# Kernel optimization log

Hardware: AMD Instinct MI355X
Metric: run time of the kernel (lower is better)

## Reference

```python
import jax, jax.numpy as jnp
import numpy as np
from jax import lax

B, T, H, W, C = 2, 32, 65, 65, 32
KS = 15   # kernel_size
F = 32    # conv features


def setup_inputs() -> dict:
    key = jax.random.key(0)
    ks = jax.random.split(key, 12)
    d = {}
    d["input_seq"] = jax.random.normal(ks[0], (B, T, H, W, C), jnp.float32)
    d["conv_w"] = jax.random.normal(ks[1], (3, 3, C, F), jnp.float32) / np.sqrt(3 * 3 * C).astype(np.float32)
    d["conv_b"] = jnp.zeros((F,), jnp.float32)
    for i, nm in enumerate(["alpha", "delta", "mu", "gamma"]):
        d[f"w_{nm}"] = jax.random.normal(ks[2 + i], (F, C), jnp.float32) / np.sqrt(F).astype(np.float32)
        d[f"b_{nm}"] = jnp.zeros((C,), jnp.float32)
    # nn.initializers.normal() -> stddev 0.01
    d["k_exc"] = jax.random.normal(ks[10], (KS, KS, C), jnp.float32) * 0.01
    d["k_inh"] = jax.random.normal(ks[11], (KS, KS, C), jnp.float32) * 0.01
    return d


def _kernel_spec(k, Hh, Ww):
    # zero-pad the (KS,KS,C) kernel to (H,W,C), then rfft2 over spatial axes
    ph, pw = (Hh - KS) // 2, (Ww - KS) // 2
    kp = jnp.pad(k, ((ph, ph), (pw, pw), (0, 0)))
    return jnp.fft.rfft2(kp, axes=(0, 1))  # (H, W//2+1, C) complex64


def reference(input_seq, conv_w, conv_b, w_alpha, b_alpha, w_delta, b_delta,
              w_mu, b_mu, w_gamma, b_gamma, k_exc, k_inh):
    Bb, Tt, Hh, Ww, Cc = input_seq.shape
    # context conv: flax Conv flattens leading (B,T) into batch; SAME, stride 2
    x = input_seq.reshape(Bb * Tt, Hh, Ww, Cc)
    stats = lax.conv_general_dilated(x, conv_w, (2, 2), 'SAME',
                                     dimension_numbers=('NHWC', 'HWIO', 'NHWC')) + conv_b
    stats = jax.nn.gelu(stats)  # flax nn.gelu (approximate)
    Hp, Wp = stats.shape[1], stats.shape[2]
    stats = stats.reshape(Bb, Tt, Hp, Wp, F)
    ctx = jnp.mean(stats, axis=(1, 2))                 # (B, Wp, F); Wp == W//2+1 for odd W
    alpha = jax.nn.sigmoid(ctx @ w_alpha + b_alpha)    # (B, Wp, C)
    delta = jax.nn.sigmoid(ctx @ w_delta + b_delta)
    mu = jax.nn.softplus(ctx @ w_mu + b_mu)
    gamma = jax.nn.softplus(ctx @ w_gamma + b_gamma)

    K_E = _kernel_spec(k_exc, Hh, Ww)  # (H, Wr, C)
    K_I = _kernel_spec(k_inh, Hh, Ww)
    Wr = Ww // 2 + 1
    decay = jnp.asarray(0.9, jnp.complex64)

    bc = lambda v: jnp.broadcast_to(v[:, None, :, :].astype(jnp.complex64), (Bb, Hh, Wr, Cc))
    A_xx = decay * bc(alpha)
    A_yy = decay * bc(delta)
    A_xy = -K_I[None] * bc(mu)
    A_yx = K_E[None] * bc(gamma)
    row0 = jnp.stack([A_xx, A_xy], axis=-1)
    row1 = jnp.stack([A_yx, A_yy], axis=-1)
    K_hat = jnp.stack([row0, row1], axis=-2)           # (B, H, Wr, C, 2, 2)

    U_hat = jnp.fft.rfft2(input_seq, axes=(2, 3))      # (B, T, H, Wr, C) complex64
    U_vec = jnp.stack([U_hat, jnp.zeros_like(U_hat)], axis=-1)  # (B,T,H,Wr,C,2)
    A_t = jnp.broadcast_to(K_hat[:, None], (Bb, Tt, Hh, Wr, Cc, 2, 2))

    # associative op for linear SSM: state_t = A_t @ state_{t-1} + u_t
    # (log/exp of the original cancel: exp(log A)=A, exp(State_log)=State)
    def combine(l, r):
        A1, b1 = l
        A2, b2 = r
        A = jnp.einsum('...ij,...jk->...ik', A2, A1)
        b = jnp.einsum('...ij,...j->...i', A2, b1) + b2
        return A, b

    _, S = lax.associative_scan(combine, (A_t, U_vec), axis=1)
    Y = S[..., 1]                                      # inhibitory component
    return jnp.fft.irfft2(Y, axes=(2, 3))              # (B, T, H, 2*(Wr-1), C) float32
```

## Files before the change

### kernel.cpp

```cpp
#include <hip/hip_runtime.h>
#include <cmath>

#define NB 2
#define NT 32
#define NH 65
#define NW 65
#define NC 32
#define NF 32
#define NKS 15
#define NHP 33
#define NWP 33
#define NWR 33
#define NWOUT 64
#define PI_F 3.14159265358979323846f

using bf16x8 = __attribute__((ext_vector_type(8))) __bf16;
using f32x4  = __attribute__((ext_vector_type(4))) float;
using s16x4  = __attribute__((ext_vector_type(4))) short;

__device__ inline unsigned short f2bf(float v) {
    unsigned u = __float_as_uint(v);
    u = u + 0x7FFF + ((u >> 16) & 1);
    return (unsigned short)(u >> 16);
}
__device__ inline float bf2f(unsigned short h) {
    return __uint_as_float((unsigned)h << 16);
}

union FragU { s16x4 h[2]; bf16x8 v; };

__global__ __launch_bounds__(256) void setup_kernel(
    const float* __restrict__ w, unsigned short* __restrict__ wBh,
    unsigned short* __restrict__ wBl,
    float2* __restrict__ twr, float2* __restrict__ twb, float2* __restrict__ twi,
    const float* __restrict__ kexc, const float* __restrict__ kinh,
    float2* __restrict__ KE, float2* __restrict__ KI)
{
    int blk = blockIdx.x;
    if (blk < 10) {
        int tid = blk * 256 + threadIdx.x;
        if (tid < NH * 36) {
            int q = tid / 36, wr = tid % 36;
            float2 v = make_float2(0.f, 0.f);
            if (wr < NWR) {
                int p = (q * wr) % NH;
                float a = -2.f * PI_F * (float)p / (float)NH;
                v = make_float2(cosf(a), sinf(a));
            }
            twr[tid] = v;
        }
        if (tid < NH * 14) {
            int h = tid / 14, b = tid % 14;
            float2 v = make_float2(0.f, 0.f);
            if (b < 13) {
                int p = (h * b) % NH;
                float a = 2.f * PI_F * (float)p / (float)NH;
                v = make_float2(cosf(a), sinf(a));
            }
            twb[tid] = v;
        }
        if (tid < 31 * 64) {
            int q = tid / 64 + 1, ow = tid % 64;
            int p = (q * ow) & 63;
            float a = 2.f * PI_F * (float)p / (float)NWOUT;
            twi[tid] = make_float2(cosf(a), sinf(a));
        }
    } else if (blk < 46) {
        int tid = (blk - 10) * 256 + threadIdx.x;
        if (tid < 9 * NF * NC) {
            int dd = tid / 1024;
            int f = (tid / 32) % 32;
            int c = tid % 32;
            float v = w[((size_t)dd * NC + c) * NF + f];
            unsigned short h = f2bf(v);
            wBh[tid] = h;
            wBl[tid] = f2bf(v - bf2f(h));
        }
    } else {
        __shared__ float2 tw[NH];
        int tid = threadIdx.x;
        if (tid < NH) {
            float a = -2.f * PI_F * (float)tid / (float)NH;
            tw[tid] = make_float2(cosf(a), sinf(a));
        }
        __syncthreads();
        int idx = (blk - 46) * 256 + tid;
        if (idx >= NH * NWR * NC) return;
        int c = idx % NC;
        int rem = idx / NC;
        int wr = rem % NWR;
        int h = rem / NWR;
        float ker = 0, kei = 0, kir = 0, kii = 0;
        int prow = (25 * (h + wr)) % NH;
        for (int i = 0; i < NKS; ++i) {
            int p = prow;
            for (int j = 0; j < NKS; ++j) {
                float2 e = tw[p];
                float ve = kexc[(i * NKS + j) * NC + c];
                float vi = kinh[(i * NKS + j) * NC + c];
                ker = fmaf(ve, e.x, ker); kei = fmaf(ve, e.y, kei);
                kir = fmaf(vi, e.x, kir); kii = fmaf(vi, e.y, kii);
                p += wr; if (p >= NH) p -= NH;
            }
            prow += h; if (prow >= NH) prow -= NH;
        }
        KE[idx] = make_float2(ker, kei);
        KI[idx] = make_float2(kir, kii);
    }
}

__global__ __launch_bounds__(256) void conv_mfma_kernel(
    const float* __restrict__ x, const unsigned short* __restrict__ wBh,
    const unsigned short* __restrict__ wBl, const float* __restrict__ bias,
    float* __restrict__ partial)
{
    __shared__ unsigned short aH[3 * 68 * 36];
    __shared__ unsigned short aL[3 * 68 * 36];
    int blk = blockIdx.x;
    int i = blk % NHP;
    int bt = blk / NHP;
    int tid = threadIdx.x;
    int l = tid & 63;
    int w = tid >> 6;

    int nt = w & 1;
    int fcol = nt * 16 + (l & 15);
    int c0 = (l >> 4) * 8;
    bf16x8 bh[9], bl[9];
    #pragma unroll
    for (int dd = 0; dd < 9; ++dd) {
        bh[dd] = *(const bf16x8*)(wBh + dd * 1024 + fcol * 32 + c0);
        bl[dd] = *(const bf16x8*)(wBl + dd * 1024 + fcol * 32 + c0);
    }

    const float* xb = x + (size_t)bt * (NH * NW * NC);
    for (int q = tid; q < 3 * 68 * 8; q += 256) {
        int r = q / 544;
        int k = q % 544;
        int pcol = k >> 3;
        int c4 = (k & 7) * 4;
        int gr = 2 * i - 1 + r;
        int gcol = pcol - 1;
        float4 v = make_float4(0.f, 0.f, 0.f, 0.f);
        if (gr >= 0 && gr < NH && gcol >= 0 && gcol < NW)
            v = *(const float4*)(xb + ((size_t)gr * NW + gcol) * NC + c4);
        int base = (r * 68 + pcol) * 36 + c4;
        unsigned short h0 = f2bf(v.x), h1 = f2bf(v.y), h2 = f2bf(v.z), h3 = f2bf(v.w);
        s16x4 th = {(short)h0, (short)h1, (short)h2, (short)h3};
        *(s16x4*)(aH + base) = th;
        s16x4 tl = {(short)f2bf(v.x - bf2f(h0)), (short)f2bf(v.y - bf2f(h1)),
                    (short)f2bf(v.z - bf2f(h2)), (short)f2bf(v.w - bf2f(h3))};
        *(s16x4*)(aL + base) = tl;
    }
    __syncthreads();

    float bv = bias[fcol];
    f32x4 acc0 = {bv, bv, bv, bv};
    f32x4 acc1 = {bv, bv, bv, bv};
    const int mtA = (w >> 1) ? 1 : 0;
    const bool hasB = (w >> 1) == 0;
    int m15 = l & 15;

    #pragma unroll
    for (int dd = 0; dd < 9; ++dd) {
        const int di = dd / 3, dj = dd % 3;
        {
            int pcol = 2 * (mtA * 16 + m15) + dj;
            int off = (di * 68 + pcol) * 36 + c0;
            FragU ah, al;
            ah.h[0] = *(const s16x4*)(aH + off);
            ah.h[1] = *(const s16x4*)(aH + off + 4);
            al.h[0] = *(const s16x4*)(aL + off);
            al.h[1] = *(const s16x4*)(aL + off + 4);
            acc0 = __builtin_amdgcn_mfma_f32_16x16x32_bf16(al.v, bh[dd], acc0, 0, 0, 0);
            acc0 = __builtin_amdgcn_mfma_f32_16x16x32_bf16(ah.v, bl[dd], acc0, 0, 0, 0);
            acc0 = __builtin_amdgcn_mfma_f32_16x16x32_bf16(ah.v, bh[dd], acc0, 0, 0, 0);
        }
        if (hasB) {
            int pcol = 2 * (32 + m15) + dj;
            if (pcol > 67) pcol = 67;
            int off = (di * 68 + pcol) * 36 + c0;
            FragU ah, al;
            ah.h[0] = *(const s16x4*)(aH + off);
            ah.h[1] = *(const s16x4*)(aH + off + 4);
            al.h[0] = *(const s16x4*)(aL + off);
            al.h[1] = *(const s16x4*)(aL + off + 4);
            acc1 = __builtin_amdgcn_mfma_f32_16x16x32_bf16(al.v, bh[dd], acc1, 0, 0, 0);
            acc1 = __builtin_amdgcn_mfma_f32_16x16x32_bf16(ah.v, bl[dd], acc1, 0, 0, 0);
            acc1 = __builtin_amdgcn_mfma_f32_16x16x32_bf16(ah.v, bh[dd], acc1, 0, 0, 0);
        }
    }

    float* pout = partial + (size_t)blk * (NWP * NF);
    int g4 = (l >> 4) * 4;
    #define GELU(v) (0.5f * (v) * (1.f + tanhf(0.7978845608028654f * ((v) + 0.044715f * (v) * (v) * (v)))))
    #pragma unroll
    for (int r = 0; r < 4; ++r) {
        float v = acc0[r];
        pout[(mtA * 16 + g4 + r) * NF + fcol] = GELU(v);
    }
    if (hasB && g4 == 0) {
        float v = acc1[0];
        pout[32 * NF + fcol] = GELU(v);
    }
    #undef GELU
}

__global__ __launch_bounds__(256) void ctx_reduce1_kernel(
    const float* __restrict__ partial, float* __restrict__ red2)
{
    __shared__ float red[4][64];
    int blk = blockIdx.x;
    int b = blk / 136;
    int rem = blk % 136;
    int chunk = rem / 8;
    int ts = rem % 8;
    int lane = threadIdx.x & 63;
    int tig = threadIdx.x >> 6;
    int jf = chunk * 64 + lane;
    float s0 = 0.f, s1 = 0.f, s2 = 0.f;
    if (jf < NWP * NF) {
        const float* p = partial + (size_t)b * (NT * NHP) * (NWP * NF)
                       + (size_t)(ts * 132 + tig * 33) * (NWP * NF) + jf;
        #pragma unroll 3
        for (int s = 0; s < 33; s += 3) {
            s0 += p[(size_t)s * (NWP * NF)];
            s1 += p[(size_t)(s + 1) * (NWP * NF)];
            s2 += p[(size_t)(s + 2) * (NWP * NF)];
        }
    }
    red[tig][lane] = s0 + s1 + s2;
    __syncthreads();
    if (threadIdx.x < 64) {
        float tot = red[0][threadIdx.x] + red[1][threadIdx.x] +
                    red[2][threadIdx.x] + red[3][threadIdx.x];
        red2[((b * 17 + chunk) * 8 + ts) * 64 + threadIdx.x] = tot;
    }
}

__global__ __launch_bounds__(256) void ctx2_gate_kernel(
    const float* __restrict__ red2,
    const float* __restrict__ wA, const float* __restrict__ bA,
    const float* __restrict__ wD, const float* __restrict__ bD,
    const float* __restrict__ wM, const float* __restrict__ bM,
    const float* __restrict__ wG, const float* __restrict__ bG,
    float* __restrict__ alpha, float* __restrict__ delta,
    float* __restrict__ mu, float* __restrict__ gamma)
{
    __shared__ float red[4][64];
    __shared__ float ctxs[64];
    int b = blockIdx.x / 17, chunk = blockIdx.x % 17;
    int lane = threadIdx.x & 63, tg = threadIdx.x >> 6;
    const float* r2 = red2 + ((size_t)(b * 17 + chunk) * 8) * 64;
    float v = r2[(2 * tg) * 64 + lane] + r2[(2 * tg + 1) * 64 + lane];
    red[tg][lane] = v;
    __syncthreads();
    if (threadIdx.x < 64) {
        int jf = chunk * 64 + threadIdx.x;
        float tot = 0.f;
        if (jf < NWP * NF)
            tot = (red[0][threadIdx.x] + red[1][threadIdx.x] +
                   red[2][threadIdx.x] + red[3][threadIdx.x]) * (1.f / (NT * NHP));
        ctxs[threadIdx.x] = tot;
    }
    __syncthreads();

    int g = threadIdx.x >> 6;
    int jl = (threadIdx.x >> 5) & 1;
    int c = threadIdx.x & 31;
    int j = chunk * 2 + jl;
    if (j < NWP) {
        const float* W  = (g == 0) ? wA : (g == 1) ? wD : (g == 2) ? wM : wG;
        const float* Bv = (g == 0) ? bA : (g == 1) ? bD : (g == 2) ? bM : bG;
        float s = Bv[c];
        #pragma unroll
        for (int f = 0; f < NF; ++f)
            s = fmaf(ctxs[jl * 32 + f], W[f * NC + c], s);
        float r;
        if (g < 2) r = 1.f / (1.f + expf(-s));
        else       r = fmaxf(s, 0.f) + log1pf(expf(-fabsf(s)));
        float* outp = (g == 0) ? alpha : (g == 1) ? delta : (g == 2) ? mu : gamma;
        outp[(b * NWP + j) * NC + c] = r;
    }
}

__global__ __launch_bounds__(256) void dft_rows_kernel(
    const float* __restrict__ x, const float2* __restrict__ twr_g,
    float2* __restrict__ U1)
{
    __shared__ __align__(16) float row[4][NW * NC];
    __shared__ __align__(16) float2 twt[NH * 36];
    int tid = threadIdx.x;
    int blk = blockIdx.x;
    int grp = blk % 17;
    int bt = blk / 17;
    int hbase = grp * 4;
    int nrows = NH - hbase; if (nrows > 4) nrows = 4;

    const float* xp = x + ((size_t)bt * NH + hbase) * (NW * NC);
    for (int idx = tid; idx < nrows * NW * NC; idx += 256) ((float*)row)[idx] = xp[idx];
    for (int idx = tid; idx < NH * 36; idx += 256) twt[idx] = twr_g[idx];
    __syncthreads();

    int c = tid & 31;
    int jg = tid >> 5;
    float2 acc[4][4];
    #pragma unroll
    for (int r = 0; r < 4; ++r)
        #pragma unroll
        for (int k = 0; k < 4; ++k) acc[r][k] = make_float2(0.f, 0.f);

    const float2* tp = twt + 4 * jg;
    #pragma unroll 5
    for (int q = 0; q < NW; ++q) {
        float4 e01 = *(const float4*)&tp[q * 36];
        float4 e23 = *(const float4*)&tp[q * 36 + 2];
        #pragma unroll
        for (int r = 0; r < 4; ++r) {
            float v = row[r][q * NC + c];
            acc[r][0].x = fmaf(v, e01.x, acc[r][0].x); acc[r][0].y = fmaf(v, e01.y, acc[r][0].y);
            acc[r][1].x = fmaf(v, e01.z, acc[r][1].x); acc[r][1].y = fmaf(v, e01.w, acc[r][1].y);
            acc[r][2].x = fmaf(v, e23.x, acc[r][2].x); acc[r][2].y = fmaf(v, e23.y, acc[r][2].y);
            acc[r][3].x = fmaf(v, e23.z, acc[r][3].x); acc[r][3].y = fmaf(v, e23.w, acc[r][3].y);
        }
    }
    #pragma unroll
    for (int r = 0; r < 4; ++r) {
        if (r < nrows) {
            float2* up = U1 + ((size_t)bt * NH + hbase + r) * (NWR * NC);
            up[(4 * jg + 0) * NC + c] = acc[r][0];
            up[(4 * jg + 1) * NC + c] = acc[r][1];
            up[(4 * jg + 2) * NC + c] = acc[r][2];
            up[(4 * jg + 3) * NC + c] = acc[r][3];
        }
    }
    if (jg == 0) {
        float2 a32[4];
        #pragma unroll
        for (int r = 0; r < 4; ++r) a32[r] = make_float2(0.f, 0.f);
        #pragma unroll 5
        for (int q = 0; q < NW; ++q) {
            float2 e = twt[q * 36 + 32];
            #pragma unroll
            for (int r = 0; r < 4; ++r) {
                float v = row[r][q * NC + c];
                a32[r].x = fmaf(v, e.x, a32[r].x);
                a32[r].y = fmaf(v, e.y, a32[r].y);
            }
        }
        #pragma unroll
        for (int r = 0; r < 4; ++r)
            if (r < nrows)
                U1[((size_t)bt * NH + hbase + r) * (NWR * NC) + 32 * NC + c] = a32[r];
    }
}

template <int SIGN>
__device__ inline void compute5(const float2 v[5], float2* outp) {
    const float C5[5] = {1.f, 0.30901699437494742f, -0.80901699437494745f,
                         -0.80901699437494745f, 0.30901699437494742f};
    const float S5[5] = {0.f, 0.95105651629515357f, 0.58778525229247314f,
                         -0.58778525229247314f, -0.95105651629515357f};
    #pragma unroll
    for (int r = 0; r < 5; ++r) {
        float re = 0.f, im = 0.f;
        #pragma unroll
        for (int a = 0; a < 5; ++a) {
            const int m = (r * a) % 5;
            const float ex = C5[m];
            const float ey = (float)SIGN * S5[m];
            re = fmaf(v[a].x, ex, fmaf(-v[a].y, ey, re));
            im = fmaf(v[a].x, ey, fmaf(v[a].y, ex, im));
        }
        outp[r * NC] = make_float2(re, im);
    }
}

template <int SIGN, bool SCALE>
__global__ __launch_bounds__(256) void dft_cols_kernel(
    const float2* __restrict__ in, float2* __restrict__ out,
    const float2* __restrict__ twb_g)
{
    __shared__ __align__(16) float2 col[NH * NC];
    __shared__ __align__(16) float2 twb[NH * 14];
    int tid = threadIdx.x;
    int blk = blockIdx.x;
    int wr = blk % NWR;
    int bt = blk / NWR;
    const float2* ip = in + ((size_t)bt * NH) * (NWR * NC) + wr * NC;
    for (int idx = tid; idx < NH * NC; idx += 256) {
        int p = idx >> 5, c = idx & 31;
        col[idx] = ip[(size_t)p * (NWR * NC) + c];
    }
    for (int idx = tid; idx < NH * 14; idx += 256) twb[idx] = twb_g[idx];
    __syncthreads();

    float2 va0[5], va1[5];
    int bq0 = tid >> 5, c0 = tid & 31;
    int q1 = tid + 256;
    int bq1 = q1 >> 5, c1 = q1 & 31;
    #pragma unroll
    for (int a = 0; a < 5; ++a) {
        va0[a] = col[(13 * a + bq0) * NC + c0];
        if (q1 < 416) va1[a] = col[(13 * a + bq1) * NC + c1];
    }
    __syncthreads();
    compute5<SIGN>(va0, &col[(bq0 * 5) * NC + c0]);
    if (q1 < 416) compute5<SIGN>(va1, &col[(bq1 * 5) * NC + c1]);
    __syncthreads();

    const float S = (float)SIGN;
    int c = tid & 31;
    int h0 = tid >> 5;
    const float s = SCALE ? (1.f / (float)NH) : 1.f;
    float2* op = out + ((size_t)bt * NH) * (NWR * NC) + wr * NC;
    float2 acc[8];
    #pragma unroll
    for (int k = 0; k < 8; ++k) {
        int h = h0 + 8 * k;
        int r = h % 5;
        const float2* Ap = col + r * NC + c;
        const float2* tp = twb + h * 14;
        float re = 0.f, im = 0.f;
        #pragma unroll
        for (int p = 0; p < 6; ++p) {
            float4 tq = *(const float4*)&tp[2 * p];
            float2 v0 = Ap[(2 * p) * 5 * NC];
            float2 v1 = Ap[(2 * p + 1) * 5 * NC];
            re = fmaf(v0.x, tq.x, fmaf(-S * v0.y, tq.y, re));
            im = fmaf(S * v0.x, tq.y, fmaf(v0.y, tq.x, im));
            re = fmaf(v1.x, tq.z, fmaf(-S * v1.y, tq.w, re));
            im = fmaf(S * v1.x, tq.w, fmaf(v1.y, tq.z, im));
        }
        {
            float2 t12 = tp[12];
            float2 v = Ap[12 * 5 * NC];
            re = fmaf(v.x, t12.x, fmaf(-S * v.y, t12.y, re));
            im = fmaf(S * v.x, t12.y, fmaf(v.y, t12.x, im));
        }
        acc[k] = make_float2(re * s, im * s);
    }
    #pragma unroll
    for (int k = 0; k < 8; ++k) {
        int h = h0 + 8 * k;
        op[(size_t)h * (NWR * NC) + c] = acc[k];
    }
    if (h0 == 0) {
        const float2* Ap = col + 4 * NC + c;
        const float2* tp = twb + 64 * 14;
        float re = 0.f, im = 0.f;
        #pragma unroll
        for (int p = 0; p < 6; ++p) {
            float4 tq = *(const float4*)&tp[2 * p];
            float2 v0 = Ap[(2 * p) * 5 * NC];
            float2 v1 = Ap[(2 * p + 1) * 5 * NC];
            re = fmaf(v0.x, tq.x, fmaf(-S * v0.y, tq.y, re));
            im = fmaf(S * v0.x, tq.y, fmaf(v0.y, tq.x, im));
            re = fmaf(v1.x, tq.z, fmaf(-S * v1.y, tq.w, re));
            im = fmaf(S * v1.x, tq.w, fmaf(v1.y, tq.z, im));
        }
        {
            float2 t12 = tp[12];
            float2 v = Ap[12 * 5 * NC];
            re = fmaf(v.x, t12.x, fmaf(-S * v.y, t12.y, re));
            im = fmaf(S * v.x, t12.y, fmaf(v.y, t12.x, im));
        }
        op[(size_t)64 * (NWR * NC) + c] = make_float2(re * s, im * s);
    }
}

__global__ __launch_bounds__(256) void scan_kernel(
    float2* __restrict__ buf, const float2* __restrict__ KE,
    const float2* __restrict__ KI, const float* __restrict__ alpha,
    const float* __restrict__ delta, const float* __restrict__ mu,
    const float* __restrict__ gamma)
{
    int idx = blockIdx.x * 256 + threadIdx.x;
    if (idx >= NB * NH * NWR * NC) return;
    int c = idx % NC;
    int rem = idx / NC;
    int wr = rem % NWR;
    int rem2 = rem / NWR;
    int h = rem2 % NH;
    int b = rem2 / NH;

    int gi = (b * NWP + wr) * NC + c;
    float axx = 0.9f * alpha[gi];
    float ayy = 0.9f * delta[gi];
    float m = mu[gi], g = gamma[gi];
    float2 ki = KI[(h * NWR + wr) * NC + c];
    float2 ke = KE[(h * NWR + wr) * NC + c];
    float2 axy = make_float2(-ki.x * m, -ki.y * m);
    float2 ayx = make_float2(ke.x * g, ke.y * g);

    float2 xs = make_float2(0.f, 0.f), ys = make_float2(0.f, 0.f);
    size_t base = ((size_t)b * NT) * NH * NWR * NC + (size_t)h * (NWR * NC) + wr * NC + c;
    const size_t stride = (size_t)NH * NWR * NC;
    for (int t = 0; t < NT; ++t) {
        float2 U = buf[base + (size_t)t * stride];
        float2 nx, ny;
        nx.x = fmaf(axx, xs.x, fmaf(axy.x, ys.x, fmaf(-axy.y, ys.y, U.x)));
        nx.y = fmaf(axx, xs.y, fmaf(axy.x, ys.y, fmaf(axy.y, ys.x, U.y)));
        ny.x = fmaf(ayx.x, xs.x, fmaf(-ayx.y, xs.y, ayy * ys.x));
        ny.y = fmaf(ayx.x, xs.y, fmaf(ayx.y, xs.x, ayy * ys.y));
        xs = nx; ys = ny;
        buf[base + (size_t)t * stride] = ys;
    }
}

__global__ __launch_bounds__(256) void irfft_w_kernel(
    const float2* __restrict__ Z, const float2* __restrict__ twi_g,
    float* __restrict__ out)
{
    __shared__ __align__(16) float2 z[4][NWR * NC];
    __shared__ __align__(16) float2 twi[31 * 64];
    int tid = threadIdx.x;
    int blk = blockIdx.x;
    int grp = blk % 17;
    int bt = blk / 17;
    int hbase = grp * 4;
    int nrows = NH - hbase; if (nrows > 4) nrows = 4;

    const float2* zp = Z + ((size_t)bt * NH + hbase) * (NWR * NC);
    for (int idx = tid; idx < nrows * NWR * NC; idx += 256) ((float2*)z)[idx] = zp[idx];
    for (int idx = tid; idx < 31 * 64; idx += 256) twi[idx] = twi_g[idx];
    __syncthreads();

    int c = tid & 31;
    int g = tid >> 5;
    float acc[4][8];
    #pragma unroll
    for (int r = 0; r < 4; ++r) {
        float z0 = z[r][c].x;
        float zn = z[r][32 * NC + c].x;
        #pragma unroll
        for (int m = 0; m < 8; ++m) acc[r][m] = z0 + ((m & 1) ? -zn : zn);
    }
    const float2* tp = twi + 8 * g;
    for (int q = 1; q < 32; ++q) {
        const float4* tq = (const float4*)&tp[(q - 1) * 64];
        float4 e0 = tq[0], e1 = tq[1], e2 = tq[2], e3 = tq[3];
        #pragma unroll
        for (int r = 0; r < 4; ++r) {
            float2 v = z[r][q * NC + c];
            float vx = 2.f * v.x, vy = 2.f * v.y;
            acc[r][0] = fmaf(vx, e0.x, fmaf(-vy, e0.y, acc[r][0]));
            acc[r][1] = fmaf(vx, e0.z, fmaf(-vy, e0.w, acc[r][1]));
            acc[r][2] = fmaf(vx, e1.x, fmaf(-vy, e1.y, acc[r][2]));
            acc[r][3] = fmaf(vx, e1.z, fmaf(-vy, e1.w, acc[r][3]));
            acc[r][4] = fmaf(vx, e2.x, fmaf(-vy, e2.y, acc[r][4]));
            acc[r][5] = fmaf(vx, e2.z, fmaf(-vy, e2.w, acc[r][5]));
            acc[r][6] = fmaf(vx, e3.x, fmaf(-vy, e3.y, acc[r][6]));
            acc[r][7] = fmaf(vx, e3.z, fmaf(-vy, e3.w, acc[r][7]));
        }
    }
    #pragma unroll
    for (int r = 0; r < 4; ++r) {
        if (r < nrows) {
            float* op = out + ((size_t)bt * NH + hbase + r) * (NWOUT * NC);
            #pragma unroll
            for (int m = 0; m < 8; ++m)
                op[(8 * g + m) * NC + c] = acc[r][m] * (1.f / (float)NWOUT);
        }
    }
}

extern "C" void kernel_launch(void* const* d_in, const int* in_sizes, int n_in,
                              void* d_out, int out_size, void* d_ws, size_t ws_size,
                              hipStream_t stream)
{
    const float* x     = (const float*)d_in[0];
    const float* convw = (const float*)d_in[1];
    const float* convb = (const float*)d_in[2];
    const float* wA = (const float*)d_in[3];
    const float* bA = (const float*)d_in[4];
    const float* wD = (const float*)d_in[5];
    const float* bD = (const float*)d_in[6];
    const float* wM = (const float*)d_in[7];
    const float* bM = (const float*)d_in[8];
    const float* wG = (const float*)d_in[9];
    const float* bG = (const float*)d_in[10];
    const float* kexc = (const float*)d_in[11];
    const float* kinh = (const float*)d_in[12];

    const size_t NBIG = (size_t)NB * NT * NH * NWR * NC;
    char* ws = (char*)d_ws;
    float2* bufA    = (float2*)ws;  ws += NBIG * sizeof(float2);
    float2* KE      = (float2*)ws;  ws += (size_t)NH * NWR * NC * sizeof(float2);
    float2* KI      = (float2*)ws;  ws += (size_t)NH * NWR * NC * sizeof(float2);
    float*  partial = (float*)ws;   ws += (size_t)NB * (NT * NHP) * (NWP * NF) * sizeof(float);
    float*  red2    = (float*)ws;   ws += (size_t)NB * 17 * 8 * 64 * sizeof(float);
    float*  alpha   = (float*)ws;   ws += (size_t)NB * NWP * NC * sizeof(float);
    float*  delta   = (float*)ws;   ws += (size_t)NB * NWP * NC * sizeof(float);
    float*  mu      = (float*)ws;   ws += (size_t)NB * NWP * NC * sizeof(float);
    float*  gamma   = (float*)ws;   ws += (size_t)NB * NWP * NC * sizeof(float);
    float2* TWR     = (float2*)ws;  ws += (size_t)NH * 36 * sizeof(float2);
    float2* TWB     = (float2*)ws;  ws += (size_t)NH * 14 * sizeof(float2);
    float2* TWI     = (float2*)ws;  ws += (size_t)31 * 64 * sizeof(float2);
    unsigned short* wBh = (unsigned short*)ws; ws += (size_t)9 * NC * NF * sizeof(unsigned short);
    unsigned short* wBl = (unsigned short*)ws; ws += (size_t)9 * NC * NF * sizeof(unsigned short);

    const int specBlocks = (NH * NWR * NC + 255) / 256;
    setup_kernel<<<46 + specBlocks, 256, 0, stream>>>(
        convw, wBh, wBl, TWR, TWB, TWI, kexc, kinh, KE, KI);

    conv_mfma_kernel<<<NB * NT * NHP, 256, 0, stream>>>(x, wBh, wBl, convb, partial);
    ctx_reduce1_kernel<<<NB * 136, 256, 0, stream>>>(partial, red2);
    ctx2_gate_kernel<<<NB * 17, 256, 0, stream>>>(
        red2, wA, bA, wD, bD, wM, bM, wG, bG, alpha, delta, mu, gamma);

    dft_rows_kernel<<<NB * NT * 17, 256, 0, stream>>>(x, TWR, bufA);
    dft_cols_kernel<-1, false><<<NB * NT * NWR, 256, 0, stream>>>(bufA, bufA, TWB);

    scan_kernel<<<(NB * NH * NWR * NC + 255) / 256, 256, 0, stream>>>(
        bufA, KE, KI, alpha, delta, mu, gamma);

    dft_cols_kernel<+1, true><<<NB * NT * NWR, 256, 0, stream>>>(bufA, bufA, TWB);
    irfft_w_kernel<<<NB * NT * 17, 256, 0, stream>>>(bufA, TWI, (float*)d_out);
}
```

Before: 165.1 us.

## Fuse column DFTs and temporal scan into one per-column kernel

Replaces the forward column DFT, the time scan and the inverse column DFT with one kernel. Each 64-thread block owns one (batch, frequency column, channel) line and loops over time: load the column, do a 5x13 factored DFT in shared memory, update the SSM state in registers, inverse-transform and write back. This removes two full read/write passes over the spectral buffer and two launches. In exchange, global accesses become strided across rows instead of coalesced over channels. Each block also runs a serial 32-step loop with four barriers per step and little occupancy, so it may become latency bound.

```diff
diff --git a/kernel.cpp b/kernel.cpp
--- a/kernel.cpp
+++ b/kernel.cpp
@@ -355,156 +355,178 @@
     }
 }
 
-template <int SIGN>
-__device__ inline void compute5(const float2 v[5], float2* outp) {
-    const float C5[5] = {1.f, 0.30901699437494742f, -0.80901699437494745f,
-                         -0.80901699437494745f, 0.30901699437494742f};
-    const float S5[5] = {0.f, 0.95105651629515357f, 0.58778525229247314f,
-                         -0.58778525229247314f, -0.95105651629515357f};
-    #pragma unroll
-    for (int r = 0; r < 5; ++r) {
-        float re = 0.f, im = 0.f;
-        #pragma unroll
-        for (int a = 0; a < 5; ++a) {
-            const int m = (r * a) % 5;
-            const float ex = C5[m];
-            const float ey = (float)SIGN * S5[m];
-            re = fmaf(v[a].x, ex, fmaf(-v[a].y, ey, re));
-            im = fmaf(v[a].x, ey, fmaf(v[a].y, ex, im));
-        }
-        outp[r * NC] = make_float2(re, im);
-    }
-}
-
-template <int SIGN, bool SCALE>
-__global__ __launch_bounds__(256) void dft_cols_kernel(
-    const float2* __restrict__ in, float2* __restrict__ out,
-    const float2* __restrict__ twb_g)
-{
-    __shared__ __align__(16) float2 col[NH * NC];
-    __shared__ __align__(16) float2 twb[NH * 14];
-    int tid = threadIdx.x;
+__global__ __launch_bounds__(64) void ssm_col_kernel(
+    float2* __restrict__ buf, const float2* __restrict__ twb_g,
+    const float2* __restrict__ KE, const float2* __restrict__ KI,
+    const float* __restrict__ alpha, const float* __restrict__ delta,
+    const float* __restrict__ mu, const float* __restrict__ gamma)
+{
+    __shared__ __align__(16) float2 colS[66];
+    __shared__ __align__(16) float2 AS[66];
+
+    const int l = threadIdx.x;
     int blk = blockIdx.x;
-    int wr = blk % NWR;
-    int bt = blk / NWR;
-    const float2* ip = in + ((size_t)bt * NH) * (NWR * NC) + wr * NC;
-    for (int idx = tid; idx < NH * NC; idx += 256) {
-        int p = idx >> 5, c = idx & 31;
-        col[idx] = ip[(size_t)p * (NWR * NC) + c];
-    }
-    for (int idx = tid; idx < NH * 14; idx += 256) twb[idx] = twb_g[idx];
-    __syncthreads();
-
-    float2 va0[5], va1[5];
-    int bq0 = tid >> 5, c0 = tid & 31;
-    int q1 = tid + 256;
-    int bq1 = q1 >> 5, c1 = q1 & 31;
-    #pragma unroll
-    for (int a = 0; a < 5; ++a) {
-        va0[a] = col[(13 * a + bq0) * NC + c0];
-        if (q1 < 416) va1[a] = col[(13 * a + bq1) * NC + c1];
-    }
-    __syncthreads();
-    compute5<SIGN>(va0, &col[(bq0 * 5) * NC + c0]);
-    if (q1 < 416) compute5<SIGN>(va1, &col[(bq1 * 5) * NC + c1]);
-    __syncthreads();
-
-    const float S = (float)SIGN;
-    int c = tid & 31;
-    int h0 = tid >> 5;
-    const float s = SCALE ? (1.f / (float)NH) : 1.f;
-    float2* op = out + ((size_t)bt * NH) * (NWR * NC) + wr * NC;
-    float2 acc[8];
-    #pragma unroll
-    for (int k = 0; k < 8; ++k) {
-        int h = h0 + 8 * k;
-        int r = h % 5;
-        const float2* Ap = col + r * NC + c;
-        const float2* tp = twb + h * 14;
-        float re = 0.f, im = 0.f;
-        #pragma unroll
-        for (int p = 0; p < 6; ++p) {
-            float4 tq = *(const float4*)&tp[2 * p];
-            float2 v0 = Ap[(2 * p) * 5 * NC];
-            float2 v1 = Ap[(2 * p + 1) * 5 * NC];
-            re = fmaf(v0.x, tq.x, fmaf(-S * v0.y, tq.y, re));
-            im = fmaf(S * v0.x, tq.y, fmaf(v0.y, tq.x, im));
-            re = fmaf(v1.x, tq.z, fmaf(-S * v1.y, tq.w, re));
-            im = fmaf(S * v1.x, tq.w, fmaf(v1.y, tq.z, im));
-        }
-        {
-            float2 t12 = tp[12];
-            float2 v = Ap[12 * 5 * NC];
-            re = fmaf(v.x, t12.x, fmaf(-S * v.y, t12.y, re));
-            im = fmaf(S * v.x, t12.y, fmaf(v.y, t12.x, im));
-        }
-        acc[k] = make_float2(re * s, im * s);
-    }
-    #pragma unroll
-    for (int k = 0; k < 8; ++k) {
-        int h = h0 + 8 * k;
-        op[(size_t)h * (NWR * NC) + c] = acc[k];
-    }
-    if (h0 == 0) {
-        const float2* Ap = col + 4 * NC + c;
-        const float2* tp = twb + 64 * 14;
-        float re = 0.f, im = 0.f;
-        #pragma unroll
-        for (int p = 0; p < 6; ++p) {
-            float4 tq = *(const float4*)&tp[2 * p];
-            float2 v0 = Ap[(2 * p) * 5 * NC];
-            float2 v1 = Ap[(2 * p + 1) * 5 * NC];
-            re = fmaf(v0.x, tq.x, fmaf(-S * v0.y, tq.y, re));
-            im = fmaf(S * v0.x, tq.y, fmaf(v0.y, tq.x, im));
-            re = fmaf(v1.x, tq.z, fmaf(-S * v1.y, tq.w, re));
-            im = fmaf(S * v1.x, tq.w, fmaf(v1.y, tq.z, im));
-        }
-        {
-            float2 t12 = tp[12];
-            float2 v = Ap[12 * 5 * NC];
-            re = fmaf(v.x, t12.x, fmaf(-S * v.y, t12.y, re));
-            im = fmaf(S * v.x, t12.y, fmaf(v.y, t12.x, im));
-        }
-        op[(size_t)64 * (NWR * NC) + c] = make_float2(re * s, im * s);
-    }
-}
-
-__global__ __launch_bounds__(256) void scan_kernel(
-    float2* __restrict__ buf, const float2* __restrict__ KE,
-    const float2* __restrict__ KI, const float* __restrict__ alpha,
-    const float* __restrict__ delta, const float* __restrict__ mu,
-    const float* __restrict__ gamma)
-{
-    int idx = blockIdx.x * 256 + threadIdx.x;
-    if (idx >= NB * NH * NWR * NC) return;
-    int c = idx % NC;
-    int rem = idx / NC;
-    int wr = rem % NWR;
-    int rem2 = rem / NWR;
-    int h = rem2 % NH;
-    int b = rem2 / NH;
+    int c = blk & 31;
+    int pair = blk >> 5;
+    int wr = pair % NWR;
+    int b = pair / NWR;
 
     int gi = (b * NWP + wr) * NC + c;
     float axx = 0.9f * alpha[gi];
     float ayy = 0.9f * delta[gi];
     float m = mu[gi], g = gamma[gi];
-    float2 ki = KI[(h * NWR + wr) * NC + c];
-    float2 ke = KE[(h * NWR + wr) * NC + c];
-    float2 axy = make_float2(-ki.x * m, -ki.y * m);
-    float2 ayx = make_float2(ke.x * g, ke.y * g);
-
-    float2 xs = make_float2(0.f, 0.f), ys = make_float2(0.f, 0.f);
-    size_t base = ((size_t)b * NT) * NH * NWR * NC + (size_t)h * (NWR * NC) + wr * NC + c;
-    const size_t stride = (size_t)NH * NWR * NC;
+
+    float2 ki0 = KI[((size_t)l * NWR + wr) * NC + c];
+    float2 ke0 = KE[((size_t)l * NWR + wr) * NC + c];
+    float2 axy0 = make_float2(-ki0.x * m, -ki0.y * m);
+    float2 ayx0 = make_float2(ke0.x * g, ke0.y * g);
+    float2 xs0 = make_float2(0.f, 0.f), ys0 = make_float2(0.f, 0.f);
+
+    float2 ki1 = KI[((size_t)64 * NWR + wr) * NC + c];
+    float2 ke1 = KE[((size_t)64 * NWR + wr) * NC + c];
+    float2 axy1 = make_float2(-ki1.x * m, -ki1.y * m);
+    float2 ayx1 = make_float2(ke1.x * g, ke1.y * g);
+    float2 xs1 = make_float2(0.f, 0.f), ys1 = make_float2(0.f, 0.f);
+
+    float2 twr0[13], twr1[13];
+    #pragma unroll
+    for (int q = 0; q < 13; ++q) {
+        twr0[q] = twb_g[l * 14 + q];
+        twr1[q] = twb_g[64 * 14 + q];
+    }
+
+    int bq = l / 5, r5 = l % 5;
+    float2 eA[5];
+    #pragma unroll
+    for (int a = 0; a < 5; ++a) {
+        int mm = (r5 * a) % 5;
+        float ang = 2.f * PI_F * 0.2f * (float)mm;
+        eA[a] = make_float2(cosf(ang), sinf(ang));
+    }
+    const float e4x[5] = {1.f, 0.30901699437494742f, -0.80901699437494745f,
+                          -0.80901699437494745f, 0.30901699437494742f};
+    const float e4y[5] = {0.f, -0.95105651629515357f, -0.58778525229247314f,
+                          0.58778525229247314f, 0.95105651629515357f};
+
+    const size_t tstride = (size_t)NH * NWR * NC;
+    const size_t hstr = (size_t)NWR * NC;
+    float2* base = buf + ((size_t)b * NT) * tstride + (size_t)wr * NC + c;
+    const float inv65 = 1.f / (float)NH;
+
     for (int t = 0; t < NT; ++t) {
-        float2 U = buf[base + (size_t)t * stride];
-        float2 nx, ny;
-        nx.x = fmaf(axx, xs.x, fmaf(axy.x, ys.x, fmaf(-axy.y, ys.y, U.x)));
-        nx.y = fmaf(axx, xs.y, fmaf(axy.x, ys.y, fmaf(axy.y, ys.x, U.y)));
-        ny.x = fmaf(ayx.x, xs.x, fmaf(-ayx.y, xs.y, ayy * ys.x));
-        ny.y = fmaf(ayx.x, xs.y, fmaf(ayx.y, xs.x, ayy * ys.y));
-        xs = nx; ys = ny;
-        buf[base + (size_t)t * stride] = ys;
+        float2* bt = base + (size_t)t * tstride;
+        float2 U = bt[(size_t)l * hstr];
+        colS[l] = U;
+        if (l == 0) colS[64] = bt[(size_t)64 * hstr];
+        __syncthreads();
+
+        {
+            float re = 0.f, im = 0.f;
+            #pragma unroll
+            for (int a = 0; a < 5; ++a) {
+                float2 v = colS[13 * a + bq];
+                re = fmaf(v.x, eA[a].x, fmaf(v.y, eA[a].y, re));
+                im = fmaf(-v.x, eA[a].y, fmaf(v.y, eA[a].x, im));
+            }
+            AS[l] = make_float2(re, im);
+            if (l == 0) {
+                float re2 = 0.f, im2 = 0.f;
+                #pragma unroll
+                for (int a = 0; a < 5; ++a) {
+                    float2 v = colS[13 * a + 12];
+                    re2 = fmaf(v.x, e4x[a], fmaf(v.y, e4y[a], re2));
+                    im2 = fmaf(-v.x, e4y[a], fmaf(v.y, e4x[a], im2));
+                }
+                AS[64] = make_float2(re2, im2);
+            }
+        }
+        __syncthreads();
+
+        {
+            float re = 0.f, im = 0.f;
+            const float2* Ap = (const float2*)AS + r5;
+            #pragma unroll
+            for (int b_ = 0; b_ < 13; ++b_) {
+                float2 e = twr0[b_];
+                float2 v = Ap[b_ * 5];
+                re = fmaf(v.x, e.x, fmaf(v.y, e.y, re));
+                im = fmaf(-v.x, e.y, fmaf(v.y, e.x, im));
+            }
+            float2 nx, ny;
+            nx.x = fmaf(axx, xs0.x, fmaf(axy0.x, ys0.x, fmaf(-axy0.y, ys0.y, re)));
+            nx.y = fmaf(axx, xs0.y, fmaf(axy0.x, ys0.y, fmaf(axy0.y, ys0.x, im)));
+            ny.x = fmaf(ayx0.x, xs0.x, fmaf(-ayx0.y, xs0.y, ayy * ys0.x));
+            ny.y = fmaf(ayx0.x, xs0.y, fmaf(ayx0.y, xs0.x, ayy * ys0.y));
+            xs0 = nx; ys0 = ny;
+            colS[l] = ny;
+            if (l == 0) {
+                float re2 = 0.f, im2 = 0.f;
+                const float2* Ap2 = (const float2*)AS + 4;
+                #pragma unroll
+                for (int b_ = 0; b_ < 13; ++b_) {
+                    float2 e = twr1[b_];
+                    float2 v = Ap2[b_ * 5];
+                    re2 = fmaf(v.x, e.x, fmaf(v.y, e.y, re2));
+                    im2 = fmaf(-v.x, e.y, fmaf(v.y, e.x, im2));
+                }
+                float2 nx2, ny2;
+                nx2.x = fmaf(axx, xs1.x, fmaf(axy1.x, ys1.x, fmaf(-axy1.y, ys1.y, re2)));
+                nx2.y = fmaf(axx, xs1.y, fmaf(axy1.x, ys1.y, fmaf(axy1.y, ys1.x, im2)));
+                ny2.x = fmaf(ayx1.x, xs1.x, fmaf(-ayx1.y, xs1.y, ayy * ys1.x));
+                ny2.y = fmaf(ayx1.x, xs1.y, fmaf(ayx1.y, xs1.x, ayy * ys1.y));
+                xs1 = nx2; ys1 = ny2;
+                colS[64] = ny2;
+            }
+        }
+        __syncthreads();
+
+        {
+            float re = 0.f, im = 0.f;
+            #pragma unroll
+            for (int a = 0; a < 5; ++a) {
+                float2 v = colS[13 * a + bq];
+                re = fmaf(v.x, eA[a].x, fmaf(-v.y, eA[a].y, re));
+                im = fmaf(v.x, eA[a].y, fmaf(v.y, eA[a].x, im));
+            }
+            AS[l] = make_float2(re, im);
+            if (l == 0) {
+                float re2 = 0.f, im2 = 0.f;
+                #pragma unroll
+                for (int a = 0; a < 5; ++a) {
+                    float2 v = colS[13 * a + 12];
+                    re2 = fmaf(v.x, e4x[a], fmaf(-v.y, e4y[a], re2));
+                    im2 = fmaf(v.x, e4y[a], fmaf(v.y, e4x[a], im2));
+                }
+                AS[64] = make_float2(re2, im2);
+            }
+        }
+        __syncthreads();
+
+        {
+            float re = 0.f, im = 0.f;
+            const float2* Ap = (const float2*)AS + r5;
+            #pragma unroll
+            for (int b_ = 0; b_ < 13; ++b_) {
+                float2 e = twr0[b_];
+                float2 v = Ap[b_ * 5];
+                re = fmaf(v.x, e.x, fmaf(-v.y, e.y, re));
+                im = fmaf(v.x, e.y, fmaf(v.y, e.x, im));
+            }
+            bt[(size_t)l * hstr] = make_float2(re * inv65, im * inv65);
+            if (l == 0) {
+                float re2 = 0.f, im2 = 0.f;
+                const float2* Ap2 = (const float2*)AS + 4;
+                #pragma unroll
+                for (int b_ = 0; b_ < 13; ++b_) {
+                    float2 e = twr1[b_];
+                    float2 v = Ap2[b_ * 5];
+                    re2 = fmaf(v.x, e.x, fmaf(-v.y, e.y, re2));
+                    im2 = fmaf(v.x, e.y, fmaf(v.y, e.x, im2));
+                }
+                bt[(size_t)64 * hstr] = make_float2(re2 * inv65, im2 * inv65);
+            }
+        }
+        __syncthreads();
     }
 }
 
@@ -610,11 +632,9 @@
         red2, wA, bA, wD, bD, wM, bM, wG, bG, alpha, delta, mu, gamma);
 
     dft_rows_kernel<<<NB * NT * 17, 256, 0, stream>>>(x, TWR, bufA);
-    dft_cols_kernel<-1, false><<<NB * NT * NWR, 256, 0, stream>>>(bufA, bufA, TWB);
-
-    scan_kernel<<<(NB * NH * NWR * NC + 255) / 256, 256, 0, stream>>>(
-        bufA, KE, KI, alpha, delta, mu, gamma);
-
-    dft_cols_kernel<+1, true><<<NB * NT * NWR, 256, 0, stream>>>(bufA, bufA, TWB);
+
+    ssm_col_kernel<<<NB * NWR * NC, 64, 0, stream>>>(
+        bufA, TWB, KE, KI, alpha, delta, mu, gamma);
+
     irfft_w_kernel<<<NB * NT * 17, 256, 0, stream>>>(bufA, TWI, (float*)d_out);
 }
```

Result: slower. 229.9 us (+39.3%).
